# Performance work log

Hardware: AMD Instinct MI355X
Metric: run time of the kernel (lower is better)

## Reference

```python
import jax, jax.numpy as jnp
import numpy as np

B, EMB, ARRAY = 4096, 512, 2
KW = KH = KC = 8
OC = 16                      # output_channel per branch
RED = OC * 2                 # SE hidden width
NUM_REL = 500
FC_IN = 3 * OC * KH * KW * KC  # 24576, flattened concat of 3 branches


def _make_chequer_perm():
    # Deterministic replication of MSLE.get_chequer_perm (perm=1).
    rng = np.random.RandomState(0)
    ent_perm = rng.permutation(EMB * (ARRAY - 1))
    rel_perm = rng.permutation(EMB)
    idxs, ei, ri = [], 0, 0
    for i in range(KC):
        for j in range(KH):
            for k in range(KW):
                for m in range(ARRAY):
                    if (i + j) % ARRAY == m:
                        idxs.append(int(rel_perm[ri]) + EMB * (ARRAY - 1)); ri += 1
                    else:
                        idxs.append(int(ent_perm[ei])); ei += 1
    return jnp.asarray(np.asarray(idxs, dtype=np.int32))


def setup_inputs() -> dict:
    key = jax.random.key(0)
    ks = jax.random.split(key, 12)
    n = lambda k, shape, s=0.05: jax.random.normal(k, shape, jnp.float32) * s
    f1_dim = ARRAY * OC * 1 * 1 * ARRAY        # (1,1,2) kernels
    f3_dim = ARRAY * OC * 1 * ARRAY * ARRAY    # (1,2,2) kernels
    f5_dim = ARRAY * OC * ARRAY * ARRAY * ARRAY  # (2,2,2) kernels
    z = lambda shape: jnp.zeros(shape, jnp.float32)
    o = lambda shape: jnp.ones(shape, jnp.float32)
    return {
        "concat_input": jax.random.normal(ks[0], (B, EMB * ARRAY), jnp.float32),
        "rel": jax.random.randint(ks[1], (B,), 0, NUM_REL),
        "chequer_perm": _make_chequer_perm(),
        "f1_table": n(ks[2], (NUM_REL, f1_dim)),
        "f3_table": n(ks[3], (NUM_REL, f3_dim)),
        "f5_table": n(ks[4], (NUM_REL, f5_dim)),
        "bn0_g": o((ARRAY,)), "bn0_b": z((ARRAY,)),
        "bn1_g": o((OC,)), "bn1_b": z((OC,)),
        "bn2_g": o((OC,)), "bn2_b": z((OC,)),
        "bn3_g": o((OC,)), "bn3_b": z((OC,)),
        "att_Wsq": n(ks[5], (OC, RED)), "att_bsq": z((RED,)),
        "att_W1": n(ks[6], (RED, OC)), "att_b1": z((OC,)),
        "att_W2": n(ks[7], (RED, OC)), "att_b2": z((OC,)),
        "att_W3": n(ks[8], (RED, OC)), "att_b3": z((OC,)),
        "fc_W": n(ks[9], (FC_IN, EMB), 0.01), "fc_b": z((EMB,)),
    }


def _bn(x, g, b, eps=1e-5):
    # BatchNorm3d, training-mode batch statistics over (N, D, H, W).
    m = x.mean(axis=(0, 2, 3, 4), keepdims=True)
    v = x.var(axis=(0, 2, 3, 4), keepdims=True)
    sh = (1, -1, 1, 1, 1)
    return (x - m) * jax.lax.rsqrt(v + eps) * g.reshape(sh) + b.reshape(sh)


def _per_sample_conv(x, w):
    # x: (B, Cin, D, H, W); w: (B, Cout, Cin, kd, kh, kw). 'same' padding,
    # even kernels pad the extra element at the high end (torch padding='same').
    conv1 = lambda xb, wb: jax.lax.conv_general_dilated(
        xb[None], wb, (1, 1, 1), 'SAME',
        dimension_numbers=('NCDHW', 'OIDHW', 'NCDHW'))[0]
    return jax.vmap(conv1)(x, w)


def reference(concat_input, rel, chequer_perm, f1_table, f3_table, f5_table,
              bn0_g, bn0_b, bn1_g, bn1_b, bn2_g, bn2_b, bn3_g, bn3_b,
              att_Wsq, att_bsq, att_W1, att_b1, att_W2, att_b2, att_W3, att_b3,
              fc_W, fc_b):
    b = concat_input.shape[0]
    # Chequered interleave of entity / relation embedding dims.
    x = concat_input[:, chequer_perm].reshape(b, ARRAY, KW, KH, KC)
    x = _bn(x, bn0_g, bn0_b)  # dropout = identity (eval)
    # Per-sample dynamic filters from relation embeddings.
    f1 = f1_table[rel].reshape(b, OC, ARRAY, 1, 1, ARRAY)
    f3 = f3_table[rel].reshape(b, OC, ARRAY, 1, ARRAY, ARRAY)
    f5 = f5_table[rel].reshape(b, OC, ARRAY, ARRAY, ARRAY, ARRAY)
    x1 = _bn(_per_sample_conv(x, f1), bn1_g, bn1_b)
    x3 = _bn(_per_sample_conv(x, f3), bn2_g, bn2_b)
    x5 = _bn(_per_sample_conv(x, f5), bn3_g, bn3_b)
    xs = x1 + x3 + x5
    # SE-style 3D attention: global pool -> shared squeeze -> 3 sigmoid gates.
    pooled = xs.mean(axis=(2, 3, 4))                       # (B, OC)
    zq = jax.nn.relu(pooled @ att_Wsq + att_bsq)           # (B, RED)
    gate = lambda W, bb: jax.nn.sigmoid(zq @ W + bb)[:, :, None, None, None]
    x1 = x1 * gate(att_W1, att_b1)
    x3 = x3 * gate(att_W2, att_b2)
    x5 = x5 * gate(att_W3, att_b3)
    out = jax.nn.relu(jnp.concatenate([x1, x3, x5], axis=1))
    out = out.reshape(b, -1)                               # (B, FC_IN)
    return out @ fc_W + fc_b                               # (B, EMB)
```

## Files before the change

kernel.cpp:

```cpp
#include <hip/hip_runtime.h>
#include <hip/hip_bf16.h>
#include <stdint.h>

typedef short s16x8 __attribute__((ext_vector_type(8)));
typedef float f32x4 __attribute__((ext_vector_type(4)));

#define NB 4096
#define KTOT 24576
#define NOUT 512
#define NCH 48

__device__ __forceinline__ short f2bf(float f){
  union { float f; uint32_t u; } x; x.f = f;
  uint32_t r = (x.u + 0x7FFFu + ((x.u >> 16) & 1u)) >> 16;
  return (short)r;
}
__device__ __forceinline__ float bf2f(short s){
  union { uint32_t u; float f; } x; x.u = ((uint32_t)(uint16_t)s) << 16;
  return x.f;
}

__global__ __launch_bounds__(256) void k_colmap(const int* __restrict__ perm,
                                                int* __restrict__ chmap,
                                                float* __restrict__ statf){
  int q = blockIdx.x * 256 + threadIdx.x;
  if (q < 1024) chmap[perm[q]] = q >> 9;
  if (blockIdx.x == 0 && threadIdx.x < 4) statf[threadIdx.x] = 0.f;
}

__global__ __launch_bounds__(256) void k_bn0(const float* __restrict__ concat,
                                             const int* __restrict__ chmap,
                                             float* __restrict__ statf){
  int t = threadIdx.x;
  float s0=0,q0=0,s1=0,q1=0;
  for (int idx = blockIdx.x*256 + t; idx < NB*1024; idx += gridDim.x*256){
    float v = concat[idx];
    int ch = chmap[idx & 1023];
    if (ch){ s1 += v; q1 += v*v; } else { s0 += v; q0 += v*v; }
  }
  #pragma unroll
  for (int m=1;m<64;m<<=1){
    s0 += __shfl_xor(s0,m); q0 += __shfl_xor(q0,m);
    s1 += __shfl_xor(s1,m); q1 += __shfl_xor(q1,m);
  }
  __shared__ float lb[4][4];
  int wid = t>>6, lane = t&63;
  if (lane==0){ lb[wid][0]=s0; lb[wid][1]=q0; lb[wid][2]=s1; lb[wid][3]=q1; }
  __syncthreads();
  if (t==0){
    float a0=0,a1=0,a2=0,a3=0;
    #pragma unroll
    for (int w=0;w<4;w++){ a0+=lb[w][0]; a1+=lb[w][1]; a2+=lb[w][2]; a3+=lb[w][3]; }
    atomicAdd(&statf[0],a0); atomicAdd(&statf[1],a1);
    atomicAdd(&statf[2],a2); atomicAdd(&statf[3],a3);
  }
}

__global__ __launch_bounds__(256) void k_wcast(const float* __restrict__ fcW,
                                               short* __restrict__ wT){
  __shared__ float tile[64][65];
  int bid = blockIdx.x;
  int kb = (bid % 384) * 64;
  int nb = (bid / 384) * 64;
  int t = threadIdx.x;
  #pragma unroll
  for (int i=0;i<16;i++){
    int r = i*4 + (t>>6), c = t & 63;
    tile[r][c] = fcW[(size_t)(kb + r)*NOUT + nb + c];
  }
  __syncthreads();
  #pragma unroll
  for (int i=0;i<16;i++){
    int n = i*4 + (t>>6), k = t & 63;
    wT[(size_t)(nb + n)*KTOT + kb + k] = f2bf(tile[k][n]);
  }
}

__global__ __launch_bounds__(256) void k_conv(
    const float* __restrict__ concat, const int* __restrict__ perm,
    const int* __restrict__ rel,
    const float* __restrict__ f1t, const float* __restrict__ f3t,
    const float* __restrict__ f5t,
    const float* __restrict__ statf,
    const float* __restrict__ bn0g, const float* __restrict__ bn0b,
    short* __restrict__ raw, float* __restrict__ psum, float* __restrict__ psq)
{
  const int b = blockIdx.x;
  const int t = threadIdx.x;
  __shared__ float xn[2*9*9*9];
  __shared__ float filt[448];
  for (int i=t;i<1458;i+=256) xn[i]=0.f;
  int r = rel[b];
  for (int i=t;i<448;i+=256){
    float v;
    if (i < 64)       v = f1t[r*64 + i];
    else if (i < 192) v = f3t[r*128 + (i-64)];
    else              v = f5t[r*256 + (i-192)];
    filt[i]=v;
  }
  __syncthreads();
  const float n0inv = 1.f/(4096.f*512.f);
  float m0 = statf[0]*n0inv, e0 = statf[1]*n0inv;
  float m1 = statf[2]*n0inv, e1 = statf[3]*n0inv;
  float sc0 = bn0g[0]*rsqrtf(e0-m0*m0+1e-5f), sh0 = bn0b[0]-m0*sc0;
  float sc1 = bn0g[1]*rsqrtf(e1-m1*m1+1e-5f), sh1 = bn0b[1]-m1*sc1;
  for (int q=t;q<1024;q+=256){
    int col = perm[q];
    float v = concat[(size_t)b*1024 + col];
    int ch = q>>9, s = q & 511;
    int d = s>>6, h=(s>>3)&7, w=s&7;
    xn[ch*729 + d*81 + h*9 + w] = ch ? v*sc1+sh1 : v*sc0+sh0;
  }
  __syncthreads();

  const int wid = t>>6, lane = t&63;
  const int d = lane>>3, h = lane&7;
  float r00[9], r01[9], r10[9], r11[9], r20[9], r21[9], r30[9], r31[9];
  #pragma unroll
  for (int w9=0;w9<9;w9++){
    int base0 = d*81 + h*9 + w9;
    int base1 = d*81 + (h+1)*9 + w9;
    int base2 = (d+1)*81 + h*9 + w9;
    int base3 = (d+1)*81 + (h+1)*9 + w9;
    r00[w9]=xn[base0];      r01[w9]=xn[729+base0];
    r10[w9]=xn[base1];      r11[w9]=xn[729+base1];
    r20[w9]=xn[base2];      r21[w9]=xn[729+base2];
    r30[w9]=xn[base3];      r31[w9]=xn[729+base3];
  }
  const size_t rawbase = (size_t)b*KTOT;

  auto finish = [&](int c, const float* v){
    float s=0,q=0;
    #pragma unroll
    for (int p=0;p<8;p++){ s += v[p]; q += v[p]*v[p]; }
    #pragma unroll
    for (int m=1;m<64;m<<=1){ s += __shfl_xor(s,m); q += __shfl_xor(q,m); }
    if (lane==0){ psum[c*NB+b]=s; psq[c*NB+b]=q; }
    s16x8 pk;
    #pragma unroll
    for (int p=0;p<8;p++) pk[p] = f2bf(v[p]);
    *reinterpret_cast<s16x8*>(raw + rawbase + (size_t)c*512 + lane*8) = pk;
  };

  #pragma unroll
  for (int i=0;i<4;i++){
    int oc = wid + 4*i;
    float c0=filt[oc*4+0], c1=filt[oc*4+1], c2=filt[oc*4+2], c3=filt[oc*4+3];
    float v[8];
    #pragma unroll
    for (int p=0;p<8;p++)
      v[p] = c0*r00[p]+c1*r00[p+1]+c2*r01[p]+c3*r01[p+1];
    finish(oc, v);
  }
  #pragma unroll
  for (int i=0;i<4;i++){
    int oc = wid + 4*i;
    const float* cf = &filt[64 + oc*8];
    float v[8];
    #pragma unroll
    for (int p=0;p<8;p++)
      v[p] = cf[0]*r00[p]+cf[1]*r00[p+1]+cf[2]*r10[p]+cf[3]*r10[p+1]
           + cf[4]*r01[p]+cf[5]*r01[p+1]+cf[6]*r11[p]+cf[7]*r11[p+1];
    finish(16+oc, v);
  }
  #pragma unroll
  for (int i=0;i<4;i++){
    int oc = wid + 4*i;
    const float* cf = &filt[192 + oc*16];
    float v[8];
    #pragma unroll
    for (int p=0;p<8;p++)
      v[p] = cf[0]*r00[p] +cf[1]*r00[p+1] +cf[2]*r10[p] +cf[3]*r10[p+1]
           + cf[4]*r20[p] +cf[5]*r20[p+1] +cf[6]*r30[p] +cf[7]*r30[p+1]
           + cf[8]*r01[p] +cf[9]*r01[p+1] +cf[10]*r11[p]+cf[11]*r11[p+1]
           + cf[12]*r21[p]+cf[13]*r21[p+1]+cf[14]*r31[p]+cf[15]*r31[p+1];
    finish(32+oc, v);
  }
}

__global__ __launch_bounds__(256) void k_bnstats(
    const float* __restrict__ psum, const float* __restrict__ psq,
    const float* __restrict__ bn1g, const float* __restrict__ bn1b,
    const float* __restrict__ bn2g, const float* __restrict__ bn2b,
    const float* __restrict__ bn3g, const float* __restrict__ bn3b,
    float* __restrict__ statf)
{
  int c = blockIdx.x, t = threadIdx.x;
  float s=0,q=0;
  for (int b=t;b<NB;b+=256){ s += psum[c*NB+b]; q += psq[c*NB+b]; }
  #pragma unroll
  for (int m=1;m<64;m<<=1){ s += __shfl_xor(s,m); q += __shfl_xor(q,m); }
  __shared__ float lb[4][2];
  int wid = t>>6, lane = t&63;
  if (lane==0){ lb[wid][0]=s; lb[wid][1]=q; }
  __syncthreads();
  if (t==0){
    s = lb[0][0]+lb[1][0]+lb[2][0]+lb[3][0];
    q = lb[0][1]+lb[1][1]+lb[2][1]+lb[3][1];
    float n = 4096.f*512.f;
    float mean = s/n, var = q/n - mean*mean;
    const float* g  = c<16 ? bn1g : (c<32 ? bn2g : bn3g);
    const float* bb = c<16 ? bn1b : (c<32 ? bn2b : bn3b);
    int oc = c & 15;
    float sc = g[oc]*rsqrtf(var + 1e-5f);
    statf[16+c] = sc;
    statf[64+c] = bb[oc] - mean*sc;
  }
}

__global__ __launch_bounds__(64) void k_se(
    const float* __restrict__ psum, const float* __restrict__ statf,
    const float* __restrict__ Wsq, const float* __restrict__ bsq,
    const float* __restrict__ W1, const float* __restrict__ b1,
    const float* __restrict__ W2, const float* __restrict__ b2,
    const float* __restrict__ W3, const float* __restrict__ b3,
    float* __restrict__ gates)
{
  int b = blockIdx.x, lane = threadIdx.x;
  __shared__ float pooled[16];
  __shared__ float zq[32];
  if (lane < 16){
    float p = 0.f;
    #pragma unroll
    for (int br=0;br<3;br++){
      int c = br*16 + lane;
      p += psum[c*NB+b]*(1.f/512.f)*statf[16+c] + statf[64+c];
    }
    pooled[lane] = p;
  }
  __syncthreads();
  if (lane < 32){
    float z = bsq[lane];
    #pragma unroll
    for (int oc=0;oc<16;oc++) z += pooled[oc]*Wsq[oc*32+lane];
    zq[lane] = fmaxf(z, 0.f);
  }
  __syncthreads();
  if (lane < 48){
    int br = lane>>4, oc = lane&15;
    const float* W  = br==0 ? W1 : (br==1 ? W2 : W3);
    const float* bb = br==0 ? b1 : (br==1 ? b2 : b3);
    float g = bb[oc];
    #pragma unroll
    for (int r2=0;r2<32;r2++) g += zq[r2]*W[r2*16+oc];
    gates[lane*NB + b] = 1.f/(1.f + expf(-g));
  }
}

__global__ __launch_bounds__(512) void k_gemm(
    const short* __restrict__ raw, const short* __restrict__ wT,
    const float* __restrict__ scale, const float* __restrict__ shift,
    const float* __restrict__ gates, float* __restrict__ partials)
{
  const int t = threadIdx.x;
  const int bid = blockIdx.x;
  const int sk = bid >> 6, rem = bid & 63;
  const int nblk = rem >> 5, mblk = rem & 31;
  const int b0 = mblk*128, n0 = nblk*256;
  const int kb0 = sk*6144;

  __shared__ short As[128][40];
  __shared__ short Ws[256][40];

  const int arow = t>>2, acol = (t&3)<<3;
  const int wrow = t>>1, wcol = (t&1)<<4;
  const short* aptr = raw + (size_t)(b0+arow)*KTOT + kb0 + acol;
  const short* wptr = wT  + (size_t)(n0+wrow)*KTOT + kb0 + wcol;

  f32x4 acc[4][4];
  #pragma unroll
  for (int m=0;m<4;m++)
    #pragma unroll
    for (int n=0;n<4;n++){ f32x4 z = {0.f,0.f,0.f,0.f}; acc[m][n]=z; }

  const int wid = t>>6, lane = t&63;
  const int wr = (wid>>2)*64, wc = (wid&3)*64;
  const int fr = lane&15, fk = (lane>>4)<<3;

  s16x8 aReg  = *reinterpret_cast<const s16x8*>(aptr);
  s16x8 wReg0 = *reinterpret_cast<const s16x8*>(wptr);
  s16x8 wReg1 = *reinterpret_cast<const s16x8*>(wptr+8);
  float gateReg = gates[(kb0>>9)*NB + b0 + arow];
  float scReg = scale[kb0>>9], shReg = shift[kb0>>9];

  for (int step=0; step<192; ++step){
    s16x8 av;
    #pragma unroll
    for (int j=0;j<8;j++){
      float x = bf2f(aReg[j]);
      x = fmaxf(x*scReg + shReg, 0.f)*gateReg;
      av[j] = f2bf(x);
    }
    *reinterpret_cast<s16x8*>(&As[arow][acol])   = av;
    *reinterpret_cast<s16x8*>(&Ws[wrow][wcol])   = wReg0;
    *reinterpret_cast<s16x8*>(&Ws[wrow][wcol+8]) = wReg1;
    if (step < 191){
      int off = (step+1)*32;
      aReg  = *reinterpret_cast<const s16x8*>(aptr + off);
      wReg0 = *reinterpret_cast<const s16x8*>(wptr + off);
      wReg1 = *reinterpret_cast<const s16x8*>(wptr + off + 8);
      int kn = kb0 + off;
      gateReg = gates[(kn>>9)*NB + b0 + arow];
      scReg = scale[kn>>9]; shReg = shift[kn>>9];
    }
    __syncthreads();
    s16x8 af[4], bfm[4];
    #pragma unroll
    for (int m=0;m<4;m++) af[m]  = *reinterpret_cast<const s16x8*>(&As[wr + m*16 + fr][fk]);
    #pragma unroll
    for (int n=0;n<4;n++) bfm[n] = *reinterpret_cast<const s16x8*>(&Ws[wc + n*16 + fr][fk]);
    #pragma unroll
    for (int m=0;m<4;m++)
      #pragma unroll
      for (int n=0;n<4;n++)
        acc[m][n] = __builtin_amdgcn_mfma_f32_16x16x32_bf16(af[m], bfm[n], acc[m][n], 0,0,0);
    __syncthreads();
  }

  float* pbase = partials + (size_t)sk*NB*NOUT;
  #pragma unroll
  for (int m=0;m<4;m++){
    #pragma unroll
    for (int j=0;j<4;j++){
      int row = b0 + wr + m*16 + (lane>>4)*4 + j;
      float* prow = pbase + (size_t)row*NOUT + n0 + wc + fr;
      #pragma unroll
      for (int n=0;n<4;n++) prow[n*16] = acc[m][n][j];
    }
  }
}

__global__ __launch_bounds__(256) void k_red(const float* __restrict__ partials,
                                             const float* __restrict__ fcb,
                                             float* __restrict__ out){
  int i = blockIdx.x*256 + threadIdx.x;
  const f32x4* p = reinterpret_cast<const f32x4*>(partials);
  f32x4 v = p[i];
  v += p[i + 524288];
  v += p[i + 2*524288];
  v += p[i + 3*524288];
  const f32x4 bias = *reinterpret_cast<const f32x4*>(fcb + ((i*4) & 511));
  v += bias;
  reinterpret_cast<f32x4*>(out)[i] = v;
}

extern "C" void kernel_launch(void* const* d_in, const int* in_sizes, int n_in,
                              void* d_out, int out_size, void* d_ws, size_t ws_size,
                              hipStream_t stream) {
  const float* concat = (const float*)d_in[0];
  const int*   rel    = (const int*)  d_in[1];
  const int*   perm   = (const int*)  d_in[2];
  const float* f1t = (const float*)d_in[3];
  const float* f3t = (const float*)d_in[4];
  const float* f5t = (const float*)d_in[5];
  const float* bn0g=(const float*)d_in[6],  *bn0b=(const float*)d_in[7];
  const float* bn1g=(const float*)d_in[8],  *bn1b=(const float*)d_in[9];
  const float* bn2g=(const float*)d_in[10], *bn2b=(const float*)d_in[11];
  const float* bn3g=(const float*)d_in[12], *bn3b=(const float*)d_in[13];
  const float* Wsq=(const float*)d_in[14],  *bsq=(const float*)d_in[15];
  const float* W1=(const float*)d_in[16],   *b1=(const float*)d_in[17];
  const float* W2=(const float*)d_in[18],   *b2=(const float*)d_in[19];
  const float* W3=(const float*)d_in[20],   *b3=(const float*)d_in[21];
  const float* fcW=(const float*)d_in[22],  *fcb=(const float*)d_in[23];
  float* out = (float*)d_out;
  char* ws = (char*)d_ws;

  const size_t off_raw  = 0;
  const size_t off_wT   = 201326592;
  const size_t off_part = 226492416;
  const size_t off_psum = 260046848;
  const size_t off_psq  = 260833280;
  const size_t off_gate = 261619712;
  const size_t off_stat = 262406144;
  const size_t off_chm  = 262406656;
  const size_t need     = off_chm + 4096;
  if (ws_size < need) return;

  short* raw      = (short*)(ws + off_raw);
  short* wT       = (short*)(ws + off_wT);
  float* partials = (float*)(ws + off_part);
  float* psum     = (float*)(ws + off_psum);
  float* psq      = (float*)(ws + off_psq);
  float* gates    = (float*)(ws + off_gate);
  float* statf    = (float*)(ws + off_stat);
  int*   chmap    = (int*)  (ws + off_chm);

  k_colmap<<<4, 256, 0, stream>>>(perm, chmap, statf);
  k_bn0   <<<2048, 256, 0, stream>>>(concat, chmap, statf);
  k_wcast <<<3072, 256, 0, stream>>>(fcW, wT);
  k_conv  <<<4096, 256, 0, stream>>>(concat, perm, rel, f1t, f3t, f5t,
                                     statf, bn0g, bn0b, raw, psum, psq);
  k_bnstats<<<48, 256, 0, stream>>>(psum, psq, bn1g, bn1b, bn2g, bn2b,
                                    bn3g, bn3b, statf);
  k_se    <<<4096, 64, 0, stream>>>(psum, statf, Wsq, bsq, W1, b1, W2, b2,
                                    W3, b3, gates);
  k_gemm  <<<256, 512, 0, stream>>>(raw, wT, statf+16, statf+64, gates, partials);
  k_red   <<<2048, 256, 0, stream>>>(partials, fcb, out);
}
```

Before: 395.0 us.

## Double-buffer GEMM with direct global-to-LDS weight loads and wider split-K

The split-K GEMM is restructured to double-buffer its LDS tiles. Weight tiles are loaded straight into swizzled LDS with global_load_lds, and the next A tile is transformed while the current MFMAs run, leaving one barrier per step instead of two. Split-K doubles from 4 to 8 (512 blocks) to fill more CUs, and the per-channel scale, shift and gate are folded and reloaded only when the channel changes. Partials are stored as bf16 to halve reduction traffic. This costs some accuracy because partial sums are rounded to bf16 before the final reduction.

```diff
diff --git a/kernel.cpp b/kernel.cpp
--- a/kernel.cpp
+++ b/kernel.cpp
@@ -3,6 +3,7 @@
 #include <stdint.h>
 
 typedef short s16x8 __attribute__((ext_vector_type(8)));
+typedef short s16x4 __attribute__((ext_vector_type(4)));
 typedef float f32x4 __attribute__((ext_vector_type(4)));
 
 #define NB 4096
@@ -19,6 +20,13 @@
   union { uint32_t u; float f; } x; x.u = ((uint32_t)(uint16_t)s) << 16;
   return x.f;
 }
+__device__ __forceinline__ short f2bf_fast(float x){
+  union { __hip_bfloat16 h; short s; } c; c.h = __float2bfloat16(x); return c.s;
+}
+
+#define GLOAD16(g, l) __builtin_amdgcn_global_load_lds( \
+  (const __attribute__((address_space(1))) void*)(g), \
+  (__attribute__((address_space(3))) void*)(l), 16, 0, 0)
 
 __global__ __launch_bounds__(256) void k_colmap(const int* __restrict__ perm,
                                                 int* __restrict__ chmap,
@@ -247,25 +255,34 @@
   }
 }
 
-__global__ __launch_bounds__(512) void k_gemm(
+__global__ __launch_bounds__(512, 4) void k_gemm(
     const short* __restrict__ raw, const short* __restrict__ wT,
     const float* __restrict__ scale, const float* __restrict__ shift,
-    const float* __restrict__ gates, float* __restrict__ partials)
+    const float* __restrict__ gates, short* __restrict__ partials)
 {
   const int t = threadIdx.x;
   const int bid = blockIdx.x;
   const int sk = bid >> 6, rem = bid & 63;
   const int nblk = rem >> 5, mblk = rem & 31;
   const int b0 = mblk*128, n0 = nblk*256;
-  const int kb0 = sk*6144;
-
-  __shared__ short As[128][40];
-  __shared__ short Ws[256][40];
+  const int kb0 = sk*3072;
+
+  __shared__ short As[2][128][40];
+  __shared__ short Ws[2][8192];
+
+  const int wid = t>>6, lane = t&63;
 
   const int arow = t>>2, acol = (t&3)<<3;
-  const int wrow = t>>1, wcol = (t&1)<<4;
   const short* aptr = raw + (size_t)(b0+arow)*KTOT + kb0 + acol;
-  const short* wptr = wT  + (size_t)(n0+wrow)*KTOT + kb0 + wcol;
+
+  const int nl0 = wid*32 + (lane>>2);
+  const int nl1 = nl0 + 16;
+  const int sl0 = (lane&3) ^ ((nl0>>1)&3);
+  const int sl1 = (lane&3) ^ ((nl1>>1)&3);
+  const short* wp0 = wT + (size_t)(n0+nl0)*KTOT + kb0 + sl0*8;
+  const short* wp1 = wT + (size_t)(n0+nl1)*KTOT + kb0 + sl1*8;
+  const int ldsw0 = wid*1024;
+  const int ldsw1 = wid*1024 + 512;
 
   f32x4 acc[4][4];
   #pragma unroll
@@ -273,75 +290,99 @@
     #pragma unroll
     for (int n=0;n<4;n++){ f32x4 z = {0.f,0.f,0.f,0.f}; acc[m][n]=z; }
 
-  const int wid = t>>6, lane = t&63;
   const int wr = (wid>>2)*64, wc = (wid&3)*64;
-  const int fr = lane&15, fk = (lane>>4)<<3;
-
-  s16x8 aReg  = *reinterpret_cast<const s16x8*>(aptr);
-  s16x8 wReg0 = *reinterpret_cast<const s16x8*>(wptr);
-  s16x8 wReg1 = *reinterpret_cast<const s16x8*>(wptr+8);
-  float gateReg = gates[(kb0>>9)*NB + b0 + arow];
-  float scReg = scale[kb0>>9], shReg = shift[kb0>>9];
-
-  for (int step=0; step<192; ++step){
+  const int fr = lane&15, fkq = lane>>4;
+
+  int wroff[4];
+  #pragma unroll
+  for (int n=0;n<4;n++){
+    int r = wc + n*16 + fr;
+    wroff[n] = r*64 + ((fkq ^ ((r>>1)&3))<<4);
+  }
+
+  GLOAD16(wp0, &Ws[0][ldsw0]);
+  GLOAD16(wp1, &Ws[0][ldsw1]);
+  s16x8 aReg = *reinterpret_cast<const s16x8*>(aptr);
+  int ch = kb0 >> 9;
+  float g = gates[ch*NB + b0 + arow];
+  float scg = scale[ch]*g, shg = shift[ch]*g;
+  {
     s16x8 av;
     #pragma unroll
-    for (int j=0;j<8;j++){
-      float x = bf2f(aReg[j]);
-      x = fmaxf(x*scReg + shReg, 0.f)*gateReg;
-      av[j] = f2bf(x);
+    for (int j=0;j<8;j++)
+      av[j] = f2bf_fast(fmaxf(bf2f(aReg[j])*scg + shg, 0.f));
+    *reinterpret_cast<s16x8*>(&As[0][arow][acol]) = av;
+  }
+  __syncthreads();
+
+  int cur = 0;
+  for (int step=0; step<96; ++step){
+    const int nxt = cur ^ 1;
+    if (step < 95){
+      const int ko = (step+1)*32;
+      GLOAD16(wp0 + ko, &Ws[nxt][ldsw0]);
+      GLOAD16(wp1 + ko, &Ws[nxt][ldsw1]);
+      aReg = *reinterpret_cast<const s16x8*>(aptr + ko);
+      int nch = (kb0 + ko) >> 9;
+      if (nch != ch){
+        ch = nch;
+        g = gates[ch*NB + b0 + arow];
+        scg = scale[ch]*g; shg = shift[ch]*g;
+      }
     }
-    *reinterpret_cast<s16x8*>(&As[arow][acol])   = av;
-    *reinterpret_cast<s16x8*>(&Ws[wrow][wcol])   = wReg0;
-    *reinterpret_cast<s16x8*>(&Ws[wrow][wcol+8]) = wReg1;
-    if (step < 191){
-      int off = (step+1)*32;
-      aReg  = *reinterpret_cast<const s16x8*>(aptr + off);
-      wReg0 = *reinterpret_cast<const s16x8*>(wptr + off);
-      wReg1 = *reinterpret_cast<const s16x8*>(wptr + off + 8);
-      int kn = kb0 + off;
-      gateReg = gates[(kn>>9)*NB + b0 + arow];
-      scReg = scale[kn>>9]; shReg = shift[kn>>9];
+    {
+      const short* asb = &As[cur][0][0];
+      const char*  wsb = (const char*)&Ws[cur][0];
+      s16x8 af[4], bfm[4];
+      #pragma unroll
+      for (int m=0;m<4;m++)
+        af[m] = *reinterpret_cast<const s16x8*>(asb + (wr + m*16 + fr)*40 + fkq*8);
+      #pragma unroll
+      for (int n=0;n<4;n++)
+        bfm[n] = *reinterpret_cast<const s16x8*>(wsb + wroff[n]);
+      #pragma unroll
+      for (int m=0;m<4;m++)
+        #pragma unroll
+        for (int n=0;n<4;n++)
+          acc[m][n] = __builtin_amdgcn_mfma_f32_16x16x32_bf16(af[m], bfm[n], acc[m][n], 0,0,0);
+    }
+    if (step < 95){
+      s16x8 av;
+      #pragma unroll
+      for (int j=0;j<8;j++)
+        av[j] = f2bf_fast(fmaxf(bf2f(aReg[j])*scg + shg, 0.f));
+      *reinterpret_cast<s16x8*>(&As[nxt][arow][acol]) = av;
     }
     __syncthreads();
-    s16x8 af[4], bfm[4];
-    #pragma unroll
-    for (int m=0;m<4;m++) af[m]  = *reinterpret_cast<const s16x8*>(&As[wr + m*16 + fr][fk]);
-    #pragma unroll
-    for (int n=0;n<4;n++) bfm[n] = *reinterpret_cast<const s16x8*>(&Ws[wc + n*16 + fr][fk]);
-    #pragma unroll
-    for (int m=0;m<4;m++)
-      #pragma unroll
-      for (int n=0;n<4;n++)
-        acc[m][n] = __builtin_amdgcn_mfma_f32_16x16x32_bf16(af[m], bfm[n], acc[m][n], 0,0,0);
-    __syncthreads();
-  }
-
-  float* pbase = partials + (size_t)sk*NB*NOUT;
+    cur = nxt;
+  }
+
+  short* pb = partials + (size_t)sk*NB*NOUT;
   #pragma unroll
   for (int m=0;m<4;m++){
     #pragma unroll
     for (int j=0;j<4;j++){
       int row = b0 + wr + m*16 + (lane>>4)*4 + j;
-      float* prow = pbase + (size_t)row*NOUT + n0 + wc + fr;
+      short* prow = pb + (size_t)row*NOUT + n0 + wc + fr;
       #pragma unroll
-      for (int n=0;n<4;n++) prow[n*16] = acc[m][n][j];
+      for (int n=0;n<4;n++) prow[n*16] = f2bf(acc[m][n][j]);
     }
   }
 }
 
-__global__ __launch_bounds__(256) void k_red(const float* __restrict__ partials,
+__global__ __launch_bounds__(256) void k_red(const short* __restrict__ partials,
                                              const float* __restrict__ fcb,
                                              float* __restrict__ out){
   int i = blockIdx.x*256 + threadIdx.x;
-  const f32x4* p = reinterpret_cast<const f32x4*>(partials);
-  f32x4 v = p[i];
-  v += p[i + 524288];
-  v += p[i + 2*524288];
-  v += p[i + 3*524288];
-  const f32x4 bias = *reinterpret_cast<const f32x4*>(fcb + ((i*4) & 511));
-  v += bias;
-  reinterpret_cast<f32x4*>(out)[i] = v;
+  int base = i*4;
+  f32x4 v = *reinterpret_cast<const f32x4*>(fcb + (base & 511));
+  #pragma unroll
+  for (int sk=0;sk<8;sk++){
+    s16x4 p = *reinterpret_cast<const s16x4*>(partials + (size_t)sk*2097152 + base);
+    v[0] += bf2f(p[0]); v[1] += bf2f(p[1]);
+    v[2] += bf2f(p[2]); v[3] += bf2f(p[3]);
+  }
+  *reinterpret_cast<f32x4*>(out + base) = v;
 }
 
 extern "C" void kernel_launch(void* const* d_in, const int* in_sizes, int n_in,
@@ -378,7 +419,7 @@
 
   short* raw      = (short*)(ws + off_raw);
   short* wT       = (short*)(ws + off_wT);
-  float* partials = (float*)(ws + off_part);
+  short* partials = (short*)(ws + off_part);
   float* psum     = (float*)(ws + off_psum);
   float* psq      = (float*)(ws + off_psq);
   float* gates    = (float*)(ws + off_gate);
@@ -394,6 +435,6 @@
                                     bn3g, bn3b, statf);
   k_se    <<<4096, 64, 0, stream>>>(psum, statf, Wsq, bsq, W1, b1, W2, b2,
                                     W3, b3, gates);
-  k_gemm  <<<256, 512, 0, stream>>>(raw, wT, statf+16, statf+64, gates, partials);
+  k_gemm  <<<512, 512, 0, stream>>>(raw, wT, statf+16, statf+64, gates, partials);
   k_red   <<<2048, 256, 0, stream>>>(partials, fcb, out);
 }
```

Result: faster. 362.7 us (-8.2%).
